# Optimization experiments

Measured on AMD Instinct MI355X. Metric: run time of the kernel, lower is better.

The kernel has to match this reference:

```python
import jax, jax.numpy as jnp
import numpy as np

N_NODES = 50000
N_EDGES = 800000


def _inv_sqrt_deg(idx, n):
    deg = jax.ops.segment_sum(jnp.ones(idx.shape, jnp.float32), idx, num_segments=n)
    return jnp.where(deg > 0, deg ** -0.5, 0.0)


def graph_conv(x, W, b, src, dst, norm_src, norm_dst):
    # DGL GraphConv, norm='both': D_dst^{-1/2} A D_src^{-1/2} X W + b
    # Apply weight before aggregation (out_feats < in_feats in both layers).
    h = (x * norm_src[:, None]) @ W            # [N, out]
    m = h[src]                                  # gather per-edge messages [E, out]
    agg = jax.ops.segment_sum(m, dst, num_segments=x.shape[0])
    return agg * norm_dst[:, None] + b


def setup_inputs() -> dict:
    key = jax.random.key(0)
    ks = jax.random.split(key, 6)
    x = jax.random.normal(ks[0], (N_NODES, 512), jnp.float32)
    W1 = jax.random.normal(ks[1], (512, 128), jnp.float32) * (512 ** -0.5)
    b1 = jnp.zeros((128,), jnp.float32)
    W2 = jax.random.normal(ks[2], (128, 40), jnp.float32) * (128 ** -0.5)
    b2 = jnp.zeros((40,), jnp.float32)
    src = jax.random.randint(ks[3], (N_EDGES,), 0, N_NODES, jnp.int32)
    dst = jax.random.randint(ks[4], (N_EDGES,), 0, N_NODES, jnp.int32)
    return {"x": x, "W1": W1, "b1": b1, "W2": W2, "b2": b2, "src": src, "dst": dst}


def reference(x, W1, b1, W2, b2, src, dst):
    n = x.shape[0]
    norm_src = _inv_sqrt_deg(src, n)  # out-degree based src norm
    norm_dst = _inv_sqrt_deg(dst, n)  # in-degree based dst norm
    h = graph_conv(x, W1, b1, src, dst, norm_src, norm_dst)
    h = jax.nn.relu(h)
    h = graph_conv(h, W2, b2, src, dst, norm_src, norm_dst)
    return h
```

## Files before the change

### kernel.cpp

```cpp
#include <hip/hip_runtime.h>
#include <hip/hip_bf16.h>

#define F0 512
#define F1 128
#define F2 40

#define NRP 12800
#define G_SL 64

typedef __attribute__((ext_vector_type(8))) short bf16x8;
typedef __attribute__((ext_vector_type(4))) float f32x4;

__device__ inline ushort f2bf(float f) {
    union { float f; uint u; } v; v.f = f;
    uint u = v.u;
    uint r = u + 0x7fffu + ((u >> 16) & 1u);
    return (ushort)(r >> 16);
}

#define CVT2(dst, a, b) { __hip_bfloat162 _t2 = __float22bfloat162_rn(make_float2(a, b)); __builtin_memcpy(&dst, &_t2, 4); }

__global__ __launch_bounds__(1024)
void hist_kernel(const int* __restrict__ src, const int* __restrict__ dst,
                 ushort* __restrict__ Gsrc, ushort* __restrict__ Gdst,
                 const float* __restrict__ W1, ushort* __restrict__ Wt, int n, int E) {
    if (blockIdx.x < (F0 * F1) / 1024) {
        int idx = blockIdx.x * 1024 + threadIdx.x;
        int k = idx >> 7, nn = idx & 127;
        Wt[nn * F0 + k] = f2bf(W1[idx]);
    }
    __shared__ uint cs[NRP / 2];
    __shared__ uint cd[NRP / 2];
    const int p = blockIdx.x / G_SL;
    const int g = blockIdx.x % G_SL;
    const int base = p * NRP;
    for (int i = threadIdx.x; i < NRP / 2; i += 1024) { cs[i] = 0; cd[i] = 0; }
    __syncthreads();
    const int Epg = (E + G_SL - 1) / G_SL;
    const int e0 = g * Epg;
    const int e1 = min(E, e0 + Epg);
    for (int i = e0 + (int)threadIdx.x; i < e1; i += 1024) {
        int s = src[i], d = dst[i];
        unsigned so = (unsigned)(s - base);
        unsigned dd = (unsigned)(d - base);
        if (so < (unsigned)NRP) atomicAdd(&cs[so >> 1], 1u << ((so & 1) * 16));
        if (dd < (unsigned)NRP) atomicAdd(&cd[dd >> 1], 1u << ((dd & 1) * 16));
    }
    __syncthreads();
    const int lim = min(NRP, n - base);
    for (int i = threadIdx.x; i < lim; i += 1024) {
        uint pcs = cs[i >> 1], pcd = cd[i >> 1];
        int sh = (i & 1) * 16;
        Gsrc[(size_t)g * n + base + i] = (ushort)((pcs >> sh) & 0xffffu);
        Gdst[(size_t)g * n + base + i] = (ushort)((pcd >> sh) & 0xffffu);
    }
}

__global__ __launch_bounds__(256)
void scanA_kernel(const ushort* __restrict__ Gsrc, const ushort* __restrict__ Gdst,
                  float* __restrict__ norm_src, float* __restrict__ norm_dst,
                  int* __restrict__ row_off, int* __restrict__ bsum, int n) {
    __shared__ int sm[256];
    int i = blockIdx.x * 256 + threadIdx.x;
    int s = 0, d = 0;
    if (i < n) {
#pragma unroll
        for (int g = 0; g < G_SL; g++) {
            s += Gsrc[(size_t)g * n + i];
            d += Gdst[(size_t)g * n + i];
        }
        norm_src[i] = s > 0 ? rsqrtf((float)s) : 0.f;
        norm_dst[i] = d > 0 ? rsqrtf((float)d) : 0.f;
    }
    sm[threadIdx.x] = (i < n) ? d : 0;
    __syncthreads();
    for (int off = 1; off < 256; off <<= 1) {
        int t = (threadIdx.x >= (unsigned)off) ? sm[threadIdx.x - off] : 0;
        __syncthreads();
        sm[threadIdx.x] += t;
        __syncthreads();
    }
    if (i < n) row_off[i + 1] = sm[threadIdx.x];
    if (threadIdx.x == 255) bsum[blockIdx.x] = sm[255];
}

__global__ __launch_bounds__(256)
void finalize_kernel(int* __restrict__ row_off, const int* __restrict__ bsum,
                     const ushort* __restrict__ Gdst, int* __restrict__ Goff, int n) {
    __shared__ int sm[256];
    const int b = blockIdx.x;
    const int t = threadIdx.x;
    sm[t] = (t < b) ? bsum[t] : 0;
    __syncthreads();
#pragma unroll
    for (int off = 128; off > 0; off >>= 1) {
        if (t < off) sm[t] += sm[t + off];
        __syncthreads();
    }
    const int excl = sm[0];
    const int v = b * 256 + t;
    if (v >= n) return;
    int raw = row_off[v];
    int start = excl + ((t == 0) ? 0 : raw);
    if (v == n - 1) {
        int rawn = row_off[n];
        row_off[n] = excl + rawn;
    }
    row_off[v] = start;
    int run = start;
#pragma unroll
    for (int g = 0; g < G_SL; g++) {
        size_t idx = (size_t)g * n + v;
        Goff[idx] = run;
        run += Gdst[idx];
    }
}

__global__ __launch_bounds__(1024)
void place_kernel(const int* __restrict__ src, const int* __restrict__ dst,
                  const int* __restrict__ Goff, int* __restrict__ edge_src, int n, int E) {
    __shared__ int cur[NRP];
    const int p = blockIdx.x / G_SL;
    const int g = blockIdx.x % G_SL;
    const int base = p * NRP;
    const int lim = min(NRP, n - base);
    for (int i = threadIdx.x; i < lim; i += 1024)
        cur[i] = Goff[(size_t)g * n + base + i];
    __syncthreads();
    const int Epg = (E + G_SL - 1) / G_SL;
    const int e0 = g * Epg;
    const int e1 = min(E, e0 + Epg);
    for (int i = e0 + (int)threadIdx.x; i < e1; i += 1024) {
        int d = dst[i];
        unsigned dd = (unsigned)(d - base);
        if (dd < (unsigned)lim) {
            int pos = atomicAdd(&cur[dd], 1);
            edge_src[pos] = src[i];
        }
    }
}

#define BM 64

#define ISSUE(kt, buf) {                                                               \
    __builtin_amdgcn_global_load_lds(                                                  \
        (const __attribute__((address_space(1))) void*)(gsrc_base + (kt) * 32),        \
        (__attribute__((address_space(3))) void*)(&Al[buf][tid * 16]),                 \
        16, 0, 0); }

#define LOADB(k0, b) { b = *reinterpret_cast<const bf16x8*>(bp + (k0)); }

#define MKFRAG(dst, mi, bufp) {                                                        \
    const int _row = (mi) * 16 + l15;                                                  \
    const char* _pr = (bufp) + _row * 128;                                             \
    float4 _pa = *reinterpret_cast<const float4*>(_pr + (((2 * lq + 0) ^ (_row & 7)) << 4)); \
    float4 _pb = *reinterpret_cast<const float4*>(_pr + (((2 * lq + 1) ^ (_row & 7)) << 4)); \
    union { uint u[4]; bf16x8 v; } _pk;                                                \
    CVT2(_pk.u[0], _pa.x, _pa.y); CVT2(_pk.u[1], _pa.z, _pa.w);                        \
    CVT2(_pk.u[2], _pb.x, _pb.y); CVT2(_pk.u[3], _pb.z, _pb.w);                        \
    dst = _pk.v; }

#define COMPUTE(buf, b) {                                                              \
    const char* _bp = &Al[buf][0];                                                     \
    bf16x8 _a0, _a1, _a2, _a3;                                                         \
    MKFRAG(_a0, 0, _bp); MKFRAG(_a1, 1, _bp); MKFRAG(_a2, 2, _bp); MKFRAG(_a3, 3, _bp);\
    acc[0] = __builtin_amdgcn_mfma_f32_16x16x32_bf16(_a0, b, acc[0], 0, 0, 0);         \
    acc[1] = __builtin_amdgcn_mfma_f32_16x16x32_bf16(_a1, b, acc[1], 0, 0, 0);         \
    acc[2] = __builtin_amdgcn_mfma_f32_16x16x32_bf16(_a2, b, acc[2], 0, 0, 0);         \
    acc[3] = __builtin_amdgcn_mfma_f32_16x16x32_bf16(_a3, b, acc[3], 0, 0, 0); }

__global__ __launch_bounds__(512)
void gemm1_mfma(const float* __restrict__ x, const ushort* __restrict__ Wt,
                const float* __restrict__ norm_src, ushort* __restrict__ h1g, int n) {
    __shared__ __align__(16) char Al[2][8192];

    const int tid = threadIdx.x;
    const int lane = tid & 63;
    const int w = tid >> 6;
    const int l15 = lane & 15;
    const int lq = lane >> 4;
    const int bm = blockIdx.x * BM;

    const int st_r = tid >> 3;
    const int st_c = (tid & 7) ^ (st_r & 7);
    int grow = bm + st_r;
    if (grow >= n) grow = n - 1;
    const float* gsrc_base = x + (size_t)grow * F0 + st_c * 4;

    const ushort* bp = Wt + (size_t)(w * 16 + l15) * F0 + lq * 8;

    f32x4 acc[4] = {};
    bf16x8 bcur, bnxt;

    ISSUE(0, 0);
    LOADB(0, bcur);
    __syncthreads();

    for (int kg = 0; kg < 16; ++kg) {
        const int cb = kg & 1;
        if (kg < 15) {
            ISSUE(kg + 1, cb ^ 1);
            LOADB((kg + 1) * 32, bnxt);
        }
        COMPUTE(cb, bcur);
        bcur = bnxt;
        if (kg < 15) __syncthreads();
    }

#pragma unroll
    for (int mi = 0; mi < 4; mi++) {
        int rbase = bm + mi * 16 + lq * 4;
#pragma unroll
        for (int r = 0; r < 4; r++) {
            int row = rbase + r;
            if (row < n) {
                float ns = norm_src[row];
                h1g[(size_t)row * F1 + w * 16 + l15] = f2bf(acc[mi][r] * ns);
            }
        }
    }
}

__global__ __launch_bounds__(256)
void agg1_kernel(const ushort* __restrict__ h1g, const int* __restrict__ row_off,
                 const int* __restrict__ edge_src, const float* __restrict__ norm_dst,
                 const float* __restrict__ b1, ushort* __restrict__ h1, int n) {
    int wid = (blockIdx.x * blockDim.x + threadIdx.x) >> 6;
    int lane = threadIdx.x & 63;
    if (wid >= n) return;
    int beg = row_off[wid], end = row_off[wid + 1];
    float a0 = 0.f, a1 = 0.f;
    int e = beg;
    for (; e + 7 < end; e += 8) {
        int s[8];
#pragma unroll
        for (int j = 0; j < 8; j++) s[j] = edge_src[e + j];
        uint v[8];
#pragma unroll
        for (int j = 0; j < 8; j++)
            v[j] = *reinterpret_cast<const uint*>(&h1g[(size_t)s[j] * F1 + lane * 2]);
#pragma unroll
        for (int j = 0; j < 8; j++) {
            a0 += __uint_as_float(v[j] << 16);
            a1 += __uint_as_float(v[j] & 0xffff0000u);
        }
    }
    for (; e < end; ++e) {
        int s = edge_src[e];
        uint v = *reinterpret_cast<const uint*>(&h1g[(size_t)s * F1 + lane * 2]);
        a0 += __uint_as_float(v << 16);
        a1 += __uint_as_float(v & 0xffff0000u);
    }
    float nd = norm_dst[wid];
    float o0 = fmaxf(a0 * nd + b1[lane * 2 + 0], 0.f);
    float o1 = fmaxf(a1 * nd + b1[lane * 2 + 1], 0.f);
    __hip_bfloat162 p2 = __float22bfloat162_rn(make_float2(o0, o1));
    uint pu; __builtin_memcpy(&pu, &p2, 4);
    *reinterpret_cast<uint*>(&h1[(size_t)wid * F1 + lane * 2]) = pu;
}

__global__ __launch_bounds__(256)
void gemm2_kernel(const ushort* __restrict__ h1, const float* __restrict__ W2,
                  const float* __restrict__ norm_src, ushort* __restrict__ h2g, int n) {
    __shared__ __align__(16) float W2s[F1][F2];
    for (int i = threadIdx.x; i < F1 * F2; i += 256)
        W2s[i / F2][i % F2] = W2[i];
    __syncthreads();
    int node = blockIdx.x * 256 + threadIdx.x;
    if (node >= n) return;
    float nrm = norm_src[node];
    f32x4 acc4[10] = {};
    const ushort* row = &h1[(size_t)node * F1];
    for (int kc = 0; kc < 16; kc++) {
        uint4 u = *reinterpret_cast<const uint4*>(&row[kc * 8]);
        uint uu[4] = {u.x, u.y, u.z, u.w};
        float f[8];
#pragma unroll
        for (int i = 0; i < 4; i++) {
            f[2 * i + 0] = __uint_as_float(uu[i] << 16);
            f[2 * i + 1] = __uint_as_float(uu[i] & 0xffff0000u);
        }
#pragma unroll
        for (int j = 0; j < 8; j++) {
#pragma unroll
            for (int c4 = 0; c4 < 10; c4++) {
                f32x4 wv = *reinterpret_cast<const f32x4*>(&W2s[kc * 8 + j][c4 * 4]);
                acc4[c4] += f[j] * wv;
            }
        }
    }
    ushort* orow = &h2g[(size_t)node * F2];
#pragma unroll
    for (int c4 = 0; c4 < 10; c4++) {
        f32x4 o = acc4[c4] * nrm;
        __hip_bfloat162 pa = __float22bfloat162_rn(make_float2(o[0], o[1]));
        __hip_bfloat162 pb = __float22bfloat162_rn(make_float2(o[2], o[3]));
        uint2 pk;
        __builtin_memcpy(&pk.x, &pa, 4);
        __builtin_memcpy(&pk.y, &pb, 4);
        *reinterpret_cast<uint2*>(&orow[c4 * 4]) = pk;
    }
}

__global__ __launch_bounds__(256)
void agg2_kernel(const ushort* __restrict__ h2g, const int* __restrict__ row_off,
                 const int* __restrict__ edge_src, const float* __restrict__ norm_dst,
                 const float* __restrict__ b2, float* __restrict__ out, int n) {
    int wid = (blockIdx.x * blockDim.x + threadIdx.x) >> 6;
    int lane = threadIdx.x & 63;
    if (wid >= n) return;
    int beg = row_off[wid], end = row_off[wid + 1];
    float a0 = 0.f, a1 = 0.f;
    int e = beg;
    const bool act = lane < 20;
    for (; e + 7 < end; e += 8) {
        int s[8];
#pragma unroll
        for (int j = 0; j < 8; j++) s[j] = edge_src[e + j];
        if (act) {
            uint v[8];
#pragma unroll
            for (int j = 0; j < 8; j++)
                v[j] = *reinterpret_cast<const uint*>(&h2g[(size_t)s[j] * F2 + lane * 2]);
#pragma unroll
            for (int j = 0; j < 8; j++) {
                a0 += __uint_as_float(v[j] << 16);
                a1 += __uint_as_float(v[j] & 0xffff0000u);
            }
        }
    }
    for (; e < end; ++e) {
        int s = edge_src[e];
        if (act) {
            uint v = *reinterpret_cast<const uint*>(&h2g[(size_t)s * F2 + lane * 2]);
            a0 += __uint_as_float(v << 16);
            a1 += __uint_as_float(v & 0xffff0000u);
        }
    }
    if (act) {
        float nd = norm_dst[wid];
        float o0 = a0 * nd + b2[lane * 2 + 0];
        float o1 = a1 * nd + b2[lane * 2 + 1];
        *reinterpret_cast<float2*>(&out[(size_t)wid * F2 + lane * 2]) = make_float2(o0, o1);
    }
}

extern "C" void kernel_launch(void* const* d_in, const int* in_sizes, int n_in,
                              void* d_out, int out_size, void* d_ws, size_t ws_size,
                              hipStream_t stream) {
    const float* x  = (const float*)d_in[0];
    const float* W1 = (const float*)d_in[1];
    const float* b1 = (const float*)d_in[2];
    const float* W2 = (const float*)d_in[3];
    const float* b2 = (const float*)d_in[4];
    const int* src  = (const int*)d_in[5];
    const int* dst  = (const int*)d_in[6];
    float* out = (float*)d_out;

    const int n = in_sizes[0] / F0;
    const int E = in_sizes[5];
    const int nb = (n + 255) / 256;
    const int P = (n + NRP - 1) / NRP;

    char* ws = (char*)d_ws;
    auto alloc = [&](size_t bytes) -> char* {
        char* p = ws;
        ws += (bytes + 255) & ~(size_t)255;
        return p;
    };
    int* row_off   = (int*)alloc((size_t)(n + 1) * 4);
    int* bsum      = (int*)alloc(256 * 4);
    int* edge_srcs = (int*)alloc((size_t)E * 4);
    float* norm_src_d = (float*)alloc((size_t)n * 4);
    float* norm_dst_d = (float*)alloc((size_t)n * 4);
    ushort* W1t = (ushort*)alloc((size_t)F1 * F0 * 2);
    ushort* h1g = (ushort*)alloc((size_t)n * F1 * 2);
    ushort* h1  = (ushort*)alloc((size_t)n * F1 * 2);
    ushort* h2g = h1g;

    ushort* Gsrc = (ushort*)h1g;
    ushort* Gdst = Gsrc + (size_t)G_SL * n;
    int* Goff = (int*)h1;

    hist_kernel<<<P * G_SL, 1024, 0, stream>>>(src, dst, Gsrc, Gdst, W1, W1t, n, E);
    scanA_kernel<<<nb, 256, 0, stream>>>(Gsrc, Gdst, norm_src_d, norm_dst_d, row_off, bsum, n);
    finalize_kernel<<<nb, 256, 0, stream>>>(row_off, bsum, Gdst, Goff, n);
    place_kernel<<<P * G_SL, 1024, 0, stream>>>(src, dst, Goff, edge_srcs, n, E);
    gemm1_mfma<<<(n + BM - 1) / BM, 512, 0, stream>>>(x, W1t, norm_src_d, h1g, n);
    agg1_kernel<<<(n + 3) / 4, 256, 0, stream>>>(h1g, row_off, edge_srcs, norm_dst_d, b1, h1, n);
    gemm2_kernel<<<(n + 255) / 256, 256, 0, stream>>>(h1, W2, norm_src_d, h2g, n);
    agg2_kernel<<<(n + 3) / 4, 256, 0, stream>>>(h2g, row_off, edge_srcs, norm_dst_d, b2, out, n);
}
```

Baseline: 179.0 us.

## Restructure gemm1 to 16-row tiles loading full K slab into LDS at once

```diff
diff --git a/kernel.cpp b/kernel.cpp
--- a/kernel.cpp
+++ b/kernel.cpp
@@ -140,83 +140,61 @@
     }
 }
 
-#define BM 64
-
-#define ISSUE(kt, buf) {                                                               \
-    __builtin_amdgcn_global_load_lds(                                                  \
-        (const __attribute__((address_space(1))) void*)(gsrc_base + (kt) * 32),        \
-        (__attribute__((address_space(3))) void*)(&Al[buf][tid * 16]),                 \
-        16, 0, 0); }
-
-#define LOADB(k0, b) { b = *reinterpret_cast<const bf16x8*>(bp + (k0)); }
-
-#define MKFRAG(dst, mi, bufp) {                                                        \
-    const int _row = (mi) * 16 + l15;                                                  \
-    const char* _pr = (bufp) + _row * 128;                                             \
-    float4 _pa = *reinterpret_cast<const float4*>(_pr + (((2 * lq + 0) ^ (_row & 7)) << 4)); \
-    float4 _pb = *reinterpret_cast<const float4*>(_pr + (((2 * lq + 1) ^ (_row & 7)) << 4)); \
-    union { uint u[4]; bf16x8 v; } _pk;                                                \
-    CVT2(_pk.u[0], _pa.x, _pa.y); CVT2(_pk.u[1], _pa.z, _pa.w);                        \
-    CVT2(_pk.u[2], _pb.x, _pb.y); CVT2(_pk.u[3], _pb.z, _pb.w);                        \
-    dst = _pk.v; }
-
-#define COMPUTE(buf, b) {                                                              \
-    const char* _bp = &Al[buf][0];                                                     \
-    bf16x8 _a0, _a1, _a2, _a3;                                                         \
-    MKFRAG(_a0, 0, _bp); MKFRAG(_a1, 1, _bp); MKFRAG(_a2, 2, _bp); MKFRAG(_a3, 3, _bp);\
-    acc[0] = __builtin_amdgcn_mfma_f32_16x16x32_bf16(_a0, b, acc[0], 0, 0, 0);         \
-    acc[1] = __builtin_amdgcn_mfma_f32_16x16x32_bf16(_a1, b, acc[1], 0, 0, 0);         \
-    acc[2] = __builtin_amdgcn_mfma_f32_16x16x32_bf16(_a2, b, acc[2], 0, 0, 0);         \
-    acc[3] = __builtin_amdgcn_mfma_f32_16x16x32_bf16(_a3, b, acc[3], 0, 0, 0); }
+#define BMR 16
 
 __global__ __launch_bounds__(512)
 void gemm1_mfma(const float* __restrict__ x, const ushort* __restrict__ Wt,
                 const float* __restrict__ norm_src, ushort* __restrict__ h1g, int n) {
-    __shared__ __align__(16) char Al[2][8192];
+    __shared__ __align__(16) char Axs[32768];
 
     const int tid = threadIdx.x;
     const int lane = tid & 63;
     const int w = tid >> 6;
     const int l15 = lane & 15;
     const int lq = lane >> 4;
-    const int bm = blockIdx.x * BM;
-
-    const int st_r = tid >> 3;
-    const int st_c = (tid & 7) ^ (st_r & 7);
-    int grow = bm + st_r;
-    if (grow >= n) grow = n - 1;
-    const float* gsrc_base = x + (size_t)grow * F0 + st_c * 4;
+    const int bm = blockIdx.x * BMR;
+
+#pragma unroll
+    for (int j = 0; j < 4; ++j) {
+        const int off = j * 8192 + tid * 16;
+        const int row = off >> 11;
+        const int slot = (off >> 4) & 127;
+        const int sslot = slot ^ (row & 7);
+        int grow = bm + row;
+        if (grow >= n) grow = n - 1;
+        const float* gsrc = x + (size_t)grow * F0 + sslot * 4;
+        __builtin_amdgcn_global_load_lds(
+            (const __attribute__((address_space(1))) void*)gsrc,
+            (__attribute__((address_space(3))) void*)(&Axs[off]),
+            16, 0, 0);
+    }
 
     const ushort* bp = Wt + (size_t)(w * 16 + l15) * F0 + lq * 8;
-
-    f32x4 acc[4] = {};
     bf16x8 bcur, bnxt;
-
-    ISSUE(0, 0);
-    LOADB(0, bcur);
-    __syncthreads();
-
-    for (int kg = 0; kg < 16; ++kg) {
-        const int cb = kg & 1;
-        if (kg < 15) {
-            ISSUE(kg + 1, cb ^ 1);
-            LOADB((kg + 1) * 32, bnxt);
-        }
-        COMPUTE(cb, bcur);
-        bcur = bnxt;
-        if (kg < 15) __syncthreads();
-    }
-
-#pragma unroll
-    for (int mi = 0; mi < 4; mi++) {
-        int rbase = bm + mi * 16 + lq * 4;
-#pragma unroll
-        for (int r = 0; r < 4; r++) {
-            int row = rbase + r;
-            if (row < n) {
-                float ns = norm_src[row];
-                h1g[(size_t)row * F1 + w * 16 + l15] = f2bf(acc[mi][r] * ns);
-            }
+    bcur = *reinterpret_cast<const bf16x8*>(bp);
+
+    __syncthreads();
+
+    f32x4 acc = {};
+#pragma unroll
+    for (int k = 0; k < 16; ++k) {
+        if (k < 15) bnxt = *reinterpret_cast<const bf16x8*>(bp + (k + 1) * 32);
+        const int c = k * 4 + lq;
+        const char* pr = &Axs[l15 * 2048];
+        float4 pa = *reinterpret_cast<const float4*>(pr + (((2 * c + 0) ^ (l15 & 7)) << 4));
+        float4 pb = *reinterpret_cast<const float4*>(pr + (((2 * c + 1) ^ (l15 & 7)) << 4));
+        union { uint u[4]; bf16x8 v; } pk;
+        CVT2(pk.u[0], pa.x, pa.y); CVT2(pk.u[1], pa.z, pa.w);
+        CVT2(pk.u[2], pb.x, pb.y); CVT2(pk.u[3], pb.z, pb.w);
+        acc = __builtin_amdgcn_mfma_f32_16x16x32_bf16(pk.v, bcur, acc, 0, 0, 0);
+        if (k < 15) bcur = bnxt;
+    }
+
+#pragma unroll
+    for (int r = 0; r < 4; ++r) {
+        int row = bm + lq * 4 + r;
+        if (row < n) {
+            h1g[(size_t)row * F1 + w * 16 + l15] = f2bf(acc[r] * norm_src[row]);
         }
     }
 }
@@ -386,7 +364,7 @@
     scanA_kernel<<<nb, 256, 0, stream>>>(Gsrc, Gdst, norm_src_d, norm_dst_d, row_off, bsum, n);
     finalize_kernel<<<nb, 256, 0, stream>>>(row_off, bsum, Gdst, Goff, n);
     place_kernel<<<P * G_SL, 1024, 0, stream>>>(src, dst, Goff, edge_srcs, n, E);
-    gemm1_mfma<<<(n + BM - 1) / BM, 512, 0, stream>>>(x, W1t, norm_src_d, h1g, n);
+    gemm1_mfma<<<(n + BMR - 1) / BMR, 512, 0, stream>>>(x, W1t, norm_src_d, h1g, n);
     agg1_kernel<<<(n + 3) / 4, 256, 0, stream>>>(h1g, row_off, edge_srcs, norm_dst_d, b1, h1, n);
     gemm2_kernel<<<(n + 255) / 256, 256, 0, stream>>>(h1, W2, norm_src_d, h2g, n);
     agg2_kernel<<<(n + 3) / 4, 256, 0, stream>>>(h2g, row_off, edge_srcs, norm_dst_d, b2, out, n);
```

After: 209.2 us. 16.9% more time.

## Shrink GEMM1 row tile with 2x2 MFMA per wave; store degree histograms as bytes

Applied to the files above, without the earlier changes.

```diff
diff --git a/kernel.cpp b/kernel.cpp
--- a/kernel.cpp
+++ b/kernel.cpp
@@ -22,7 +22,7 @@
 
 __global__ __launch_bounds__(1024)
 void hist_kernel(const int* __restrict__ src, const int* __restrict__ dst,
-                 ushort* __restrict__ Gsrc, ushort* __restrict__ Gdst,
+                 uchar* __restrict__ Gsrc, uchar* __restrict__ Gdst,
                  const float* __restrict__ W1, ushort* __restrict__ Wt, int n, int E) {
     if (blockIdx.x < (F0 * F1) / 1024) {
         int idx = blockIdx.x * 1024 + threadIdx.x;
@@ -51,13 +51,13 @@
     for (int i = threadIdx.x; i < lim; i += 1024) {
         uint pcs = cs[i >> 1], pcd = cd[i >> 1];
         int sh = (i & 1) * 16;
-        Gsrc[(size_t)g * n + base + i] = (ushort)((pcs >> sh) & 0xffffu);
-        Gdst[(size_t)g * n + base + i] = (ushort)((pcd >> sh) & 0xffffu);
-    }
-}
-
-__global__ __launch_bounds__(256)
-void scanA_kernel(const ushort* __restrict__ Gsrc, const ushort* __restrict__ Gdst,
+        Gsrc[(size_t)g * n + base + i] = (uchar)((pcs >> sh) & 0xffu);
+        Gdst[(size_t)g * n + base + i] = (uchar)((pcd >> sh) & 0xffu);
+    }
+}
+
+__global__ __launch_bounds__(256)
+void scanA_kernel(const uchar* __restrict__ Gsrc, const uchar* __restrict__ Gdst,
                   float* __restrict__ norm_src, float* __restrict__ norm_dst,
                   int* __restrict__ row_off, int* __restrict__ bsum, int n) {
     __shared__ int sm[256];
@@ -86,7 +86,7 @@
 
 __global__ __launch_bounds__(256)
 void finalize_kernel(int* __restrict__ row_off, const int* __restrict__ bsum,
-                     const ushort* __restrict__ Gdst, int* __restrict__ Goff, int n) {
+                     const uchar* __restrict__ Gdst, int* __restrict__ Goff, int n) {
     __shared__ int sm[256];
     const int b = blockIdx.x;
     const int t = threadIdx.x;
@@ -140,7 +140,7 @@
     }
 }
 
-#define BM 64
+#define BM 32
 
 #define ISSUE(kt, buf) {                                                               \
     __builtin_amdgcn_global_load_lds(                                                  \
@@ -148,7 +148,9 @@
         (__attribute__((address_space(3))) void*)(&Al[buf][tid * 16]),                 \
         16, 0, 0); }
 
-#define LOADB(k0, b) { b = *reinterpret_cast<const bf16x8*>(bp + (k0)); }
+#define LOADB(k0) {                                                                    \
+    bnxt0 = *reinterpret_cast<const bf16x8*>(bp0 + (k0));                              \
+    bnxt1 = *reinterpret_cast<const bf16x8*>(bp1 + (k0)); }
 
 #define MKFRAG(dst, mi, bufp) {                                                        \
     const int _row = (mi) * 16 + l15;                                                  \
@@ -160,19 +162,19 @@
     CVT2(_pk.u[2], _pb.x, _pb.y); CVT2(_pk.u[3], _pb.z, _pb.w);                        \
     dst = _pk.v; }
 
-#define COMPUTE(buf, b) {                                                              \
+#define COMPUTE(buf, b0, b1) {                                                         \
     const char* _bp = &Al[buf][0];                                                     \
-    bf16x8 _a0, _a1, _a2, _a3;                                                         \
-    MKFRAG(_a0, 0, _bp); MKFRAG(_a1, 1, _bp); MKFRAG(_a2, 2, _bp); MKFRAG(_a3, 3, _bp);\
-    acc[0] = __builtin_amdgcn_mfma_f32_16x16x32_bf16(_a0, b, acc[0], 0, 0, 0);         \
-    acc[1] = __builtin_amdgcn_mfma_f32_16x16x32_bf16(_a1, b, acc[1], 0, 0, 0);         \
-    acc[2] = __builtin_amdgcn_mfma_f32_16x16x32_bf16(_a2, b, acc[2], 0, 0, 0);         \
-    acc[3] = __builtin_amdgcn_mfma_f32_16x16x32_bf16(_a3, b, acc[3], 0, 0, 0); }
-
-__global__ __launch_bounds__(512)
+    bf16x8 _a0, _a1;                                                                   \
+    MKFRAG(_a0, 0, _bp); MKFRAG(_a1, 1, _bp);                                          \
+    acc[0][0] = __builtin_amdgcn_mfma_f32_16x16x32_bf16(_a0, b0, acc[0][0], 0, 0, 0);  \
+    acc[0][1] = __builtin_amdgcn_mfma_f32_16x16x32_bf16(_a0, b1, acc[0][1], 0, 0, 0);  \
+    acc[1][0] = __builtin_amdgcn_mfma_f32_16x16x32_bf16(_a1, b0, acc[1][0], 0, 0, 0);  \
+    acc[1][1] = __builtin_amdgcn_mfma_f32_16x16x32_bf16(_a1, b1, acc[1][1], 0, 0, 0); }
+
+__global__ __launch_bounds__(256)
 void gemm1_mfma(const float* __restrict__ x, const ushort* __restrict__ Wt,
                 const float* __restrict__ norm_src, ushort* __restrict__ h1g, int n) {
-    __shared__ __align__(16) char Al[2][8192];
+    __shared__ __align__(16) char Al[2][4096];
 
     const int tid = threadIdx.x;
     const int lane = tid & 63;
@@ -187,35 +189,40 @@
     if (grow >= n) grow = n - 1;
     const float* gsrc_base = x + (size_t)grow * F0 + st_c * 4;
 
-    const ushort* bp = Wt + (size_t)(w * 16 + l15) * F0 + lq * 8;
-
-    f32x4 acc[4] = {};
-    bf16x8 bcur, bnxt;
+    const ushort* bp0 = Wt + (size_t)(w * 32 + 0 + l15) * F0 + lq * 8;
+    const ushort* bp1 = Wt + (size_t)(w * 32 + 16 + l15) * F0 + lq * 8;
+
+    f32x4 acc[2][2] = {};
+    bf16x8 bcur0, bcur1, bnxt0, bnxt1;
 
     ISSUE(0, 0);
-    LOADB(0, bcur);
+    LOADB(0);
+    bcur0 = bnxt0; bcur1 = bnxt1;
     __syncthreads();
 
     for (int kg = 0; kg < 16; ++kg) {
         const int cb = kg & 1;
         if (kg < 15) {
             ISSUE(kg + 1, cb ^ 1);
-            LOADB((kg + 1) * 32, bnxt);
-        }
-        COMPUTE(cb, bcur);
-        bcur = bnxt;
+            LOADB((kg + 1) * 32);
+        }
+        COMPUTE(cb, bcur0, bcur1);
+        bcur0 = bnxt0; bcur1 = bnxt1;
         if (kg < 15) __syncthreads();
     }
 
 #pragma unroll
-    for (int mi = 0; mi < 4; mi++) {
+    for (int mi = 0; mi < 2; mi++) {
         int rbase = bm + mi * 16 + lq * 4;
 #pragma unroll
         for (int r = 0; r < 4; r++) {
             int row = rbase + r;
             if (row < n) {
                 float ns = norm_src[row];
-                h1g[(size_t)row * F1 + w * 16 + l15] = f2bf(acc[mi][r] * ns);
+#pragma unroll
+                for (int ni = 0; ni < 2; ni++) {
+                    h1g[(size_t)row * F1 + w * 32 + ni * 16 + l15] = f2bf(acc[mi][ni][r] * ns);
+                }
             }
         }
     }
@@ -378,15 +385,15 @@
     ushort* h1  = (ushort*)alloc((size_t)n * F1 * 2);
     ushort* h2g = h1g;
 
-    ushort* Gsrc = (ushort*)h1g;
-    ushort* Gdst = Gsrc + (size_t)G_SL * n;
+    uchar* Gsrc = (uchar*)h1g;
+    uchar* Gdst = Gsrc + (size_t)G_SL * n;
     int* Goff = (int*)h1;
 
     hist_kernel<<<P * G_SL, 1024, 0, stream>>>(src, dst, Gsrc, Gdst, W1, W1t, n, E);
     scanA_kernel<<<nb, 256, 0, stream>>>(Gsrc, Gdst, norm_src_d, norm_dst_d, row_off, bsum, n);
     finalize_kernel<<<nb, 256, 0, stream>>>(row_off, bsum, Gdst, Goff, n);
     place_kernel<<<P * G_SL, 1024, 0, stream>>>(src, dst, Goff, edge_srcs, n, E);
-    gemm1_mfma<<<(n + BM - 1) / BM, 512, 0, stream>>>(x, W1t, norm_src_d, h1g, n);
+    gemm1_mfma<<<(n + BM - 1) / BM, 256, 0, stream>>>(x, W1t, norm_src_d, h1g, n);
     agg1_kernel<<<(n + 3) / 4, 256, 0, stream>>>(h1g, row_off, edge_srcs, norm_dst_d, b1, h1, n);
     gemm2_kernel<<<(n + 255) / 256, 256, 0, stream>>>(h1, W2, norm_src_d, h2g, n);
     agg2_kernel<<<(n + 3) / 4, 256, 0, stream>>>(h2g, row_off, edge_srcs, norm_dst_d, b2, out, n);
```

Result: slower. 188.7 us (+5.4%).

## Fuse edge placement into GEMM1 launch and shrink degree histograms to bytes

Applied to the files above, without the earlier changes.

```diff
diff --git a/kernel.cpp b/kernel.cpp
--- a/kernel.cpp
+++ b/kernel.cpp
@@ -22,7 +22,7 @@
 
 __global__ __launch_bounds__(1024)
 void hist_kernel(const int* __restrict__ src, const int* __restrict__ dst,
-                 ushort* __restrict__ Gsrc, ushort* __restrict__ Gdst,
+                 uchar* __restrict__ Gsrc, uchar* __restrict__ Gdst,
                  const float* __restrict__ W1, ushort* __restrict__ Wt, int n, int E) {
     if (blockIdx.x < (F0 * F1) / 1024) {
         int idx = blockIdx.x * 1024 + threadIdx.x;
@@ -51,13 +51,13 @@
     for (int i = threadIdx.x; i < lim; i += 1024) {
         uint pcs = cs[i >> 1], pcd = cd[i >> 1];
         int sh = (i & 1) * 16;
-        Gsrc[(size_t)g * n + base + i] = (ushort)((pcs >> sh) & 0xffffu);
-        Gdst[(size_t)g * n + base + i] = (ushort)((pcd >> sh) & 0xffffu);
+        Gsrc[(size_t)g * n + base + i] = (uchar)((pcs >> sh) & 0xffu);
+        Gdst[(size_t)g * n + base + i] = (uchar)((pcd >> sh) & 0xffu);
     }
 }
 
 __global__ __launch_bounds__(256)
-void scanA_kernel(const ushort* __restrict__ Gsrc, const ushort* __restrict__ Gdst,
+void scanA_kernel(const uchar* __restrict__ Gsrc, const uchar* __restrict__ Gdst,
                   float* __restrict__ norm_src, float* __restrict__ norm_dst,
                   int* __restrict__ row_off, int* __restrict__ bsum, int n) {
     __shared__ int sm[256];
@@ -86,7 +86,7 @@
 
 __global__ __launch_bounds__(256)
 void finalize_kernel(int* __restrict__ row_off, const int* __restrict__ bsum,
-                     const ushort* __restrict__ Gdst, int* __restrict__ Goff, int n) {
+                     const uchar* __restrict__ Gdst, int* __restrict__ Goff, int n) {
     __shared__ int sm[256];
     const int b = blockIdx.x;
     const int t = threadIdx.x;
@@ -116,36 +116,17 @@
     }
 }
 
-__global__ __launch_bounds__(1024)
-void place_kernel(const int* __restrict__ src, const int* __restrict__ dst,
-                  const int* __restrict__ Goff, int* __restrict__ edge_src, int n, int E) {
-    __shared__ int cur[NRP];
-    const int p = blockIdx.x / G_SL;
-    const int g = blockIdx.x % G_SL;
-    const int base = p * NRP;
-    const int lim = min(NRP, n - base);
-    for (int i = threadIdx.x; i < lim; i += 1024)
-        cur[i] = Goff[(size_t)g * n + base + i];
-    __syncthreads();
-    const int Epg = (E + G_SL - 1) / G_SL;
-    const int e0 = g * Epg;
-    const int e1 = min(E, e0 + Epg);
-    for (int i = e0 + (int)threadIdx.x; i < e1; i += 1024) {
-        int d = dst[i];
-        unsigned dd = (unsigned)(d - base);
-        if (dd < (unsigned)lim) {
-            int pos = atomicAdd(&cur[dd], 1);
-            edge_src[pos] = src[i];
-        }
-    }
-}
-
 #define BM 64
+
+union SmemU {
+    int cur[NRP];
+    char Al[2][8192];
+};
 
 #define ISSUE(kt, buf) {                                                               \
     __builtin_amdgcn_global_load_lds(                                                  \
         (const __attribute__((address_space(1))) void*)(gsrc_base + (kt) * 32),        \
-        (__attribute__((address_space(3))) void*)(&Al[buf][tid * 16]),                 \
+        (__attribute__((address_space(3))) void*)(&smu.Al[buf][tid * 16]),             \
         16, 0, 0); }
 
 #define LOADB(k0, b) { b = *reinterpret_cast<const bf16x8*>(bp + (k0)); }
@@ -161,7 +142,7 @@
     dst = _pk.v; }
 
 #define COMPUTE(buf, b) {                                                              \
-    const char* _bp = &Al[buf][0];                                                     \
+    const char* _bp = &smu.Al[buf][0];                                                 \
     bf16x8 _a0, _a1, _a2, _a3;                                                         \
     MKFRAG(_a0, 0, _bp); MKFRAG(_a1, 1, _bp); MKFRAG(_a2, 2, _bp); MKFRAG(_a3, 3, _bp);\
     acc[0] = __builtin_amdgcn_mfma_f32_16x16x32_bf16(_a0, b, acc[0], 0, 0, 0);         \
@@ -170,11 +151,37 @@
     acc[3] = __builtin_amdgcn_mfma_f32_16x16x32_bf16(_a3, b, acc[3], 0, 0, 0); }
 
 __global__ __launch_bounds__(512)
-void gemm1_mfma(const float* __restrict__ x, const ushort* __restrict__ Wt,
-                const float* __restrict__ norm_src, ushort* __restrict__ h1g, int n) {
-    __shared__ __align__(16) char Al[2][8192];
-
+void place_gemm1_fused(const int* __restrict__ src, const int* __restrict__ dst,
+                       const int* __restrict__ Goff, int* __restrict__ edge_src,
+                       const float* __restrict__ x, const ushort* __restrict__ Wt,
+                       const float* __restrict__ norm_src, ushort* __restrict__ h1g,
+                       int n, int E, int ngemm) {
+    __shared__ __align__(16) SmemU smu;
     const int tid = threadIdx.x;
+
+    if (blockIdx.x >= ngemm) {
+        const int pb = blockIdx.x - ngemm;
+        const int p = pb / G_SL;
+        const int g = pb % G_SL;
+        const int base = p * NRP;
+        const int lim = min(NRP, n - base);
+        for (int i = tid; i < lim; i += 512)
+            smu.cur[i] = Goff[(size_t)g * n + base + i];
+        __syncthreads();
+        const int Epg = (E + G_SL - 1) / G_SL;
+        const int e0 = g * Epg;
+        const int e1 = min(E, e0 + Epg);
+        for (int i = e0 + tid; i < e1; i += 512) {
+            int d = dst[i];
+            unsigned dd = (unsigned)(d - base);
+            if (dd < (unsigned)lim) {
+                int pos = atomicAdd(&smu.cur[dd], 1);
+                edge_src[pos] = src[i];
+            }
+        }
+        return;
+    }
+
     const int lane = tid & 63;
     const int w = tid >> 6;
     const int l15 = lane & 15;
@@ -361,6 +368,7 @@
     const int E = in_sizes[5];
     const int nb = (n + 255) / 256;
     const int P = (n + NRP - 1) / NRP;
+    const int ngemm = (n + BM - 1) / BM;
 
     char* ws = (char*)d_ws;
     auto alloc = [&](size_t bytes) -> char* {
@@ -378,15 +386,15 @@
     ushort* h1  = (ushort*)alloc((size_t)n * F1 * 2);
     ushort* h2g = h1g;
 
-    ushort* Gsrc = (ushort*)h1g;
-    ushort* Gdst = Gsrc + (size_t)G_SL * n;
+    uchar* Gsrc = (uchar*)h1g;
+    uchar* Gdst = Gsrc + (size_t)G_SL * n;
     int* Goff = (int*)h1;
 
     hist_kernel<<<P * G_SL, 1024, 0, stream>>>(src, dst, Gsrc, Gdst, W1, W1t, n, E);
     scanA_kernel<<<nb, 256, 0, stream>>>(Gsrc, Gdst, norm_src_d, norm_dst_d, row_off, bsum, n);
     finalize_kernel<<<nb, 256, 0, stream>>>(row_off, bsum, Gdst, Goff, n);
-    place_kernel<<<P * G_SL, 1024, 0, stream>>>(src, dst, Goff, edge_srcs, n, E);
-    gemm1_mfma<<<(n + BM - 1) / BM, 512, 0, stream>>>(x, W1t, norm_src_d, h1g, n);
+    place_gemm1_fused<<<ngemm + P * G_SL, 512, 0, stream>>>(
+        src, dst, Goff, edge_srcs, x, W1t, norm_src_d, h1g, n, E, ngemm);
     agg1_kernel<<<(n + 3) / 4, 256, 0, stream>>>(h1g, row_off, edge_srcs, norm_dst_d, b1, h1, n);
     gemm2_kernel<<<(n + 255) / 256, 256, 0, stream>>>(h1, W2, norm_src_d, h2g, n);
     agg2_kernel<<<(n + 3) / 4, 256, 0, stream>>>(h2g, row_off, edge_srcs, norm_dst_d, b2, out, n);
```

Measured after the change: 175.8 us, median of 3. No clear change (-1.8%).
